# Kernel tuning notes

Measured on AMD Instinct MI355X. Metric: run time of the kernel, lower is better.

Reference implementation:

```python
import jax, jax.numpy as jnp
import numpy as np

VOCAB_SIZE = 512


def setup_inputs() -> dict:
    key = jax.random.key(0)
    k1, k2, k3 = jax.random.split(key, 3)
    B, S, W = 64, 512, 24
    sents = jax.random.randint(k1, (B, S, W), 0, VOCAB_SIZE, dtype=jnp.int64)
    lengths = jax.random.randint(k2, (B,), 1, S, dtype=jnp.int64)
    alpha = jax.random.uniform(k3, (1,), dtype=jnp.float32)  # forgetting_factor param
    return {"sents": sents, "lengths": lengths, "alpha": alpha}


def reference(sents, lengths, alpha):
    # FOFE recurrence z = alpha*z + onehot(char), applied ONLY at non-pad chars
    # (char_id == 0 leaves z unchanged). Closed form: each non-pad char k
    # contributes alpha^(number of non-pad chars strictly after k) to bin char_k.
    a = alpha[0]
    m = (sents != 0).astype(a.dtype)                      # [B,S,W] non-pad mask
    csum = jnp.cumsum(m, axis=-1)                         # inclusive cumsum
    suffix = csum[..., -1:] - csum                        # #non-pad chars after k
    w = m * jnp.power(a, suffix)                          # [B,S,W] decay weights
    B, S, W = sents.shape
    b = jnp.arange(B)[:, None, None]
    s = jnp.arange(S)[None, :, None]
    out = jnp.zeros((B, S, VOCAB_SIZE), dtype=w.dtype)
    out = out.at[b, s, sents].add(w)                      # scatter-accumulate
    return (out, lengths)
```

## Files before the change

kernel.cpp:

```cpp
#include <hip/hip_runtime.h>

#define VOCAB 512
#define W 24
#define WAVES_PER_BLOCK 4

__global__ __launch_bounds__(256, 8) void fofe_kernel(
    const int*   __restrict__ sents,
    const int*   __restrict__ lengths,
    const float* __restrict__ alpha_p,
    float*       __restrict__ out,
    int nrows, int nlen)
{
    __shared__ float lds[WAVES_PER_BLOCK][VOCAB];

    const int wave  = threadIdx.x >> 6;
    const int lane  = threadIdx.x & 63;
    const int gwave = blockIdx.x * WAVES_PER_BLOCK + wave;
    const int nw    = gridDim.x * WAVES_PER_BLOCK;
    const float alpha = alpha_p[0];

    if (blockIdx.x == 0 && threadIdx.x < nlen) {
        out[(size_t)nrows * VOCAB + threadIdx.x] = (float)lengths[threadIdx.x];
    }

    float*  bins  = lds[wave];
    float4* bins4 = (float4*)bins;

    for (int row = gwave; row < nrows; row += nw) {
        const float4 z = make_float4(0.f, 0.f, 0.f, 0.f);
        bins4[lane]      = z;
        bins4[lane + 64] = z;

        int c = 0;
        if (lane < W) c = sents[(size_t)row * W + lane];

        unsigned long long mask = __ballot(c != 0);
        if (c != 0) {
            int suffix = __popcll(mask >> (lane + 1));
            float acc = 1.0f, p = alpha;
            #pragma unroll
            for (int b = 0; b < 5; ++b) {
                if (suffix & (1 << b)) acc *= p;
                p *= p;
            }
            atomicAdd(&bins[c], acc);
        }

        asm volatile("s_waitcnt lgkmcnt(0)" ::: "memory");

        float4* out4 = (float4*)(out + (size_t)row * VOCAB);
        out4[lane]      = bins4[lane];
        out4[lane + 64] = bins4[lane + 64];
    }
}

extern "C" void kernel_launch(void* const* d_in, const int* in_sizes, int n_in,
                              void* d_out, int out_size, void* d_ws, size_t ws_size,
                              hipStream_t stream) {
    const int*   sents   = (const int*)d_in[0];
    const int*   lengths = (const int*)d_in[1];
    const float* alpha   = (const float*)d_in[2];
    float*       out     = (float*)d_out;

    const int nrows = in_sizes[0] / W;
    const int nlen  = in_sizes[1];

    int blocks = 2048;
    int max_blocks = (nrows + WAVES_PER_BLOCK - 1) / WAVES_PER_BLOCK;
    if (blocks > max_blocks) blocks = max_blocks;
    fofe_kernel<<<blocks, 256, 0, stream>>>(sents, lengths, alpha, out, nrows, nlen);
}
```

Before: 79.46 us.

## Batch four rows per wave with prefetched loads, double LDS bins, nontemporal stores

Each wave now handles exactly four rows. It loads all four rows' character ids up front and computes the decay weights for all of them before any scatter, so the global load latency overlaps. Bins are double-buffered in LDS so two rows are scattered and written out per pass, and output uses nontemporal stores to avoid cache pollution on the write-only output. The grid is sized exactly to rows/16 instead of capping at 2048 blocks, which costs twice the LDS per wave and more registers.

```diff
diff --git a/kernel.cpp b/kernel.cpp
--- a/kernel.cpp
+++ b/kernel.cpp
@@ -2,7 +2,10 @@
 
 #define VOCAB 512
 #define W 24
-#define WAVES_PER_BLOCK 4
+#define WPB 4
+#define RPW 4
+
+typedef float f32x4 __attribute__((ext_vector_type(4)));
 
 __global__ __launch_bounds__(256, 8) void fofe_kernel(
     const int*   __restrict__ sents,
@@ -11,46 +14,65 @@
     float*       __restrict__ out,
     int nrows, int nlen)
 {
-    __shared__ float lds[WAVES_PER_BLOCK][VOCAB];
+    __shared__ float lds[WPB][2][VOCAB];
 
     const int wave  = threadIdx.x >> 6;
     const int lane  = threadIdx.x & 63;
-    const int gwave = blockIdx.x * WAVES_PER_BLOCK + wave;
-    const int nw    = gridDim.x * WAVES_PER_BLOCK;
-    const float alpha = alpha_p[0];
+    const int gwave = blockIdx.x * WPB + wave;
+    const int nw    = gridDim.x * WPB;
 
     if (blockIdx.x == 0 && threadIdx.x < nlen) {
         out[(size_t)nrows * VOCAB + threadIdx.x] = (float)lengths[threadIdx.x];
     }
 
-    float*  bins  = lds[wave];
-    float4* bins4 = (float4*)bins;
+    const float alpha = alpha_p[0];
 
-    for (int row = gwave; row < nrows; row += nw) {
-        const float4 z = make_float4(0.f, 0.f, 0.f, 0.f);
-        bins4[lane]      = z;
-        bins4[lane + 64] = z;
+    int rows[RPW];
+    int c[RPW];
+    #pragma unroll
+    for (int k = 0; k < RPW; ++k) {
+        rows[k] = gwave + k * nw;
+        c[k] = 0;
+        if (rows[k] < nrows && lane < W)
+            c[k] = sents[(size_t)rows[k] * W + lane];
+    }
 
-        int c = 0;
-        if (lane < W) c = sents[(size_t)row * W + lane];
+    float w[RPW];
+    #pragma unroll
+    for (int k = 0; k < RPW; ++k) {
+        unsigned long long mask = __ballot(c[k] != 0);
+        int suffix = __popcll(mask >> ((lane + 1) & 63));
+        float acc = 1.0f, p = alpha;
+        #pragma unroll
+        for (int b = 0; b < 5; ++b) { if (suffix & (1 << b)) acc *= p; p *= p; }
+        w[k] = acc;
+    }
 
-        unsigned long long mask = __ballot(c != 0);
-        if (c != 0) {
-            int suffix = __popcll(mask >> (lane + 1));
-            float acc = 1.0f, p = alpha;
-            #pragma unroll
-            for (int b = 0; b < 5; ++b) {
-                if (suffix & (1 << b)) acc *= p;
-                p *= p;
-            }
-            atomicAdd(&bins[c], acc);
-        }
+    f32x4* b04 = (f32x4*)lds[wave][0];
+    f32x4* b14 = (f32x4*)lds[wave][1];
+    float* b0  = (float*)b04;
+    float* b1  = (float*)b14;
 
+    #pragma unroll
+    for (int pair = 0; pair < RPW / 2; ++pair) {
+        const int k0 = 2 * pair, k1 = 2 * pair + 1;
+        const f32x4 z = (f32x4)(0.f);
+        b04[lane] = z; b04[lane + 64] = z;
+        b14[lane] = z; b14[lane + 64] = z;
+        if (c[k0] != 0) atomicAdd(&b0[c[k0]], w[k0]);
+        if (c[k1] != 0) atomicAdd(&b1[c[k1]], w[k1]);
         asm volatile("s_waitcnt lgkmcnt(0)" ::: "memory");
 
-        float4* out4 = (float4*)(out + (size_t)row * VOCAB);
-        out4[lane]      = bins4[lane];
-        out4[lane + 64] = bins4[lane + 64];
+        if (rows[k0] < nrows) {
+            f32x4* o = (f32x4*)(out + (size_t)rows[k0] * VOCAB);
+            __builtin_nontemporal_store(b04[lane],      &o[lane]);
+            __builtin_nontemporal_store(b04[lane + 64], &o[lane + 64]);
+        }
+        if (rows[k1] < nrows) {
+            f32x4* o = (f32x4*)(out + (size_t)rows[k1] * VOCAB);
+            __builtin_nontemporal_store(b14[lane],      &o[lane]);
+            __builtin_nontemporal_store(b14[lane + 64], &o[lane + 64]);
+        }
     }
 }
 
@@ -65,8 +87,6 @@
     const int nrows = in_sizes[0] / W;
     const int nlen  = in_sizes[1];
 
-    int blocks = 2048;
-    int max_blocks = (nrows + WAVES_PER_BLOCK - 1) / WAVES_PER_BLOCK;
-    if (blocks > max_blocks) blocks = max_blocks;
+    int blocks = (nrows + WPB * RPW - 1) / (WPB * RPW);
     fofe_kernel<<<blocks, 256, 0, stream>>>(sents, lengths, alpha, out, nrows, nlen);
 }
```

Result: no change. 79.84 us (+0.5%).
